# Performance work log

Measured on AMD Instinct MI355X. Metric: run time of the kernel, lower is better.

The kernel has to match this reference:

```python
import jax, jax.numpy as jnp
import numpy as np

N = 100000   # nodes
E = 1600000  # edges
H = 128      # hidden_channels
G = 2        # group
D = H // G   # per-group channels
L = 2        # num_layers
T = 112      # num_tasks
MSG_EPS = 1e-7


def _ln(x, g, b):
    mu = jnp.mean(x, axis=-1, keepdims=True)
    var = jnp.var(x, axis=-1, keepdims=True)
    return (x - mu) * jax.lax.rsqrt(var + 1e-5) * g + b


def setup_inputs() -> dict:
    key = jax.random.key(0)
    ks = jax.random.split(key, 12)
    s8, s16, sH, sD = 1/np.sqrt(8), 1/np.sqrt(16), 1/np.sqrt(H), 1/np.sqrt(D)
    inp = {}
    inp["x"] = jax.random.uniform(ks[0], (N, 8), jnp.float32)
    inp["node_index"] = jax.random.randint(ks[1], (N,), 0, N)
    inp["edge_index"] = jax.random.randint(ks[2], (2, E), 0, N)
    inp["edge_attr"] = jax.random.uniform(ks[3], (E, 8), jnp.float32)
    inp["node_features"] = jax.random.normal(ks[4], (N, 8), jnp.float32)
    inp["W_oh"] = jax.random.normal(ks[5], (8, 8)) * s8
    inp["b_oh"] = jnp.zeros((8,))
    inp["W_ne"] = jax.random.normal(ks[6], (16, H)) * s16
    inp["b_ne"] = jnp.zeros((H,))
    inp["W_ee"] = jax.random.normal(ks[7], (8, H)) * s8
    inp["b_ee"] = jnp.zeros((H,))
    inp["ln_g"] = jnp.ones((L, G, D))
    inp["ln_b"] = jnp.zeros((L, G, D))
    inp["We"] = jax.random.normal(ks[8], (L, G, H, D)) * sH   # GENConv edge encoder per Fm
    inp["be"] = jnp.zeros((L, G, D))
    inp["Wm"] = jax.random.normal(ks[9], (L, G, D, D)) * sD   # GENConv 1-layer MLP
    inp["bm"] = jnp.zeros((L, G, D))
    inp["last_g"] = jnp.ones((H,))
    inp["last_b"] = jnp.zeros((H,))
    inp["Wp"] = jax.random.normal(ks[10], (H, T)) * sH
    inp["bp"] = jnp.zeros((T,))
    return inp


def _gen_block(y_in, src, dst, ee, g, b, We_, be_, Wm_, bm_):
    # GENBlock (res+ pre-activation): norm -> relu -> GENConv(softmax aggr, t=1)
    h = jax.nn.relu(_ln(y_in, g, b))                       # [N,D]
    msg = jax.nn.relu(h[src] + ee @ We_ + be_) + MSG_EPS   # [E,D]
    mx = jax.lax.stop_gradient(jax.ops.segment_max(msg, dst, num_segments=N))
    mx = jnp.where(jnp.isfinite(mx), mx, 0.0)
    ex = jnp.exp(msg - mx[dst])
    den = jax.ops.segment_sum(ex, dst, num_segments=N)
    w = ex / (den[dst] + 1e-16)                            # scatter_softmax weights
    agg = jax.ops.segment_sum(msg * w, dst, num_segments=N)  # [N,D]
    return (h + agg) @ Wm_ + bm_


def reference(x, node_index, edge_index, edge_attr, node_features, W_oh, b_oh, W_ne, b_ne, W_ee, b_ee, ln_g, ln_b, We, be, Wm, bm, last_g, last_b, Wp, bp):
    nf1 = node_features[node_index]                        # [N,8]
    nf2 = x @ W_oh + b_oh                                  # one-hot encoder [N,8]
    h = jnp.concatenate([nf1, nf2], axis=1) @ W_ne + b_ne  # [N,H]
    ee = edge_attr @ W_ee + b_ee                           # [E,H]; cat of G copies chunks back to identical [E,H]
    src, dst = edge_index[0], edge_index[1]
    for l in range(L):
        # GroupAdditiveCoupling (group=2): y_i = x_i + F_i(y_{i-1})
        x1, x2 = jnp.split(h, G, axis=-1)
        y1 = x1 + _gen_block(x2, src, dst, ee, ln_g[l, 0], ln_b[l, 0], We[l, 0], be[l, 0], Wm[l, 0], bm[l, 0])
        y2 = x2 + _gen_block(y1, src, dst, ee, ln_g[l, 1], ln_b[l, 1], We[l, 1], be[l, 1], Wm[l, 1], bm[l, 1])
        h = jnp.concatenate([y1, y2], axis=-1)
    h = jax.nn.relu(_ln(h, last_g, last_b))
    return h @ Wp + bp
```

## Files before the change

### kernel.cpp

```cpp
#include <hip/hip_runtime.h>

constexpr int N_NODES = 100000;
constexpr int N_EDGES = 1600000;
constexpr int T_OUT = 112;

constexpr int SCAN_CHUNK = 1024;
constexpr int SCAN_BLOCKS = (N_NODES + SCAN_CHUNK - 1) / SCAN_CHUNK;

typedef _Float16 h2v __attribute__((ext_vector_type(2)));
typedef _Float16 half8 __attribute__((ext_vector_type(8)));
typedef float f32x4 __attribute__((ext_vector_type(4)));
typedef int i4v __attribute__((ext_vector_type(4)));
typedef float f4v __attribute__((ext_vector_type(4)));

__device__ __forceinline__ float dot2h(h2v a, h2v b, float c) {
#if __has_builtin(__builtin_amdgcn_fdot2)
    return __builtin_amdgcn_fdot2(a, b, c, false);
#else
    return fmaf((float)a.x, (float)b.x, fmaf((float)a.y, (float)b.y, c));
#endif
}
__device__ __forceinline__ int pk2(float a, float b) {
    auto v = __builtin_amdgcn_cvt_pkrtz(a, b);
    return __builtin_bit_cast(int, v);
}
__device__ __forceinline__ h2v b2h(int x) { return __builtin_bit_cast(h2v, x); }
__device__ __forceinline__ unsigned short f2h(float f) {
    return __builtin_bit_cast(unsigned short, (_Float16)f);
}

__global__ void wcomb_kernel(const float* __restrict__ W_ee,
                             const float* __restrict__ b_ee,
                             const float* __restrict__ We,
                             const float* __restrict__ be,
                             int* __restrict__ Wc_h2,
                             float* __restrict__ bcomb) {
    int lg = blockIdx.x;
    int d = threadIdx.x;
    const float* We_ = We + (size_t)lg * 128 * 64;
    float acc[9];
#pragma unroll
    for (int k = 0; k < 9; ++k) acc[k] = 0.f;
    for (int c = 0; c < 128; ++c) {
        float wv = We_[c * 64 + d];
#pragma unroll
        for (int k = 0; k < 8; ++k) acc[k] += W_ee[k * 128 + c] * wv;
        acc[8] += b_ee[c] * wv;
    }
#pragma unroll
    for (int j = 0; j < 4; ++j)
        Wc_h2[lg * 256 + j * 64 + d] = pk2(acc[2 * j], acc[2 * j + 1]);
    bcomb[lg * 64 + d] = acc[8] + be[lg * 64 + d];
}

__global__ void wp_pack_kernel(const float* __restrict__ Wp, int* __restrict__ wpfrag) {
    int tm = blockIdx.x;
    int tile = tm >> 2, m = tm & 3;
    int lane = threadIdx.x;
    int g = lane >> 4, r = lane & 15;
    int t = tile * 16 + r;
    int o[4];
#pragma unroll
    for (int p = 0; p < 4; ++p) {
        int j0 = 2 * p, j1 = 2 * p + 1;
        int k0 = m * 32 + (j0 >> 2) * 16 + g * 4 + (j0 & 3);
        int k1 = m * 32 + (j1 >> 2) * 16 + g * 4 + (j1 & 3);
        o[p] = pk2(Wp[k0 * 112 + t], Wp[k1 * 112 + t]);
    }
    int4 o4; o4.x = o[0]; o4.y = o[1]; o4.z = o[2]; o4.w = o[3];
    *(int4*)(wpfrag + ((size_t)tm * 64 + lane) * 4) = o4;
}

__global__ void wm_pack_kernel(const float* __restrict__ Wm, int* __restrict__ wmfrag) {
    int b = blockIdx.x;
    int lg = b >> 3, tm = b & 7;
    int tile = tm >> 1, m = tm & 1;
    int lane = threadIdx.x;
    int g = lane >> 4, r = lane & 15;
    const float* W = Wm + (size_t)lg * 4096;
    int col = tile * 16 + r;
    int o[4];
#pragma unroll
    for (int p = 0; p < 4; ++p) {
        int j0 = 2 * p, j1 = 2 * p + 1;
        int k0 = m * 32 + (j0 >> 2) * 16 + g * 4 + (j0 & 3);
        int k1 = m * 32 + (j1 >> 2) * 16 + g * 4 + (j1 & 3);
        o[p] = pk2(W[k0 * 64 + col], W[k1 * 64 + col]);
    }
    int4 o4; o4.x = o[0]; o4.y = o[1]; o4.z = o[2]; o4.w = o[3];
    *(int4*)(wmfrag + ((size_t)b * 64 + lane) * 4) = o4;
}

__global__ __launch_bounds__(256) void encoder_kernel(
    const float* __restrict__ x, const int* __restrict__ node_index,
    const float* __restrict__ node_features,
    const float* __restrict__ W_oh, const float* __restrict__ b_oh,
    const float* __restrict__ W_ne, const float* __restrict__ b_ne,
    float* __restrict__ A, float* __restrict__ B) {
    int tid = threadIdx.x;
    int w = tid >> 6, d = tid & 63;
    int n = blockIdx.x * 4 + w;

    float xf[8];
    const float* xr = x + (size_t)n * 8;
#pragma unroll
    for (int j = 0; j < 8; ++j) xf[j] = xr[j];

    float nf[16];
    int ni = node_index[n];
    const float* nfr = node_features + (size_t)ni * 8;
#pragma unroll
    for (int k = 0; k < 8; ++k) nf[k] = nfr[k];
#pragma unroll
    for (int k = 0; k < 8; ++k) {
        float acc = b_oh[k];
#pragma unroll
        for (int j = 0; j < 8; ++j) acc += xf[j] * W_oh[j * 8 + k];
        nf[8 + k] = acc;
    }
    float hA = b_ne[d], hB = b_ne[64 + d];
#pragma unroll
    for (int k = 0; k < 16; ++k) {
        hA += nf[k] * W_ne[k * 128 + d];
        hB += nf[k] * W_ne[k * 128 + 64 + d];
    }
    A[(size_t)n * 64 + d] = hA;
    B[(size_t)n * 64 + d] = hB;
}

__global__ void hist_kernel(const int* __restrict__ edge_index,
                            int* __restrict__ deg, int* __restrict__ rank) {
    int e = blockIdx.x * 256 + threadIdx.x;
    if (e < N_EDGES) rank[e] = atomicAdd(&deg[edge_index[N_EDGES + e]], 1);
}

__global__ __launch_bounds__(256) void block_sum_kernel(const int* __restrict__ deg,
                                                        int* __restrict__ blocksum) {
    __shared__ int s_w[4];
    int t = threadIdx.x;
    int base = blockIdx.x * SCAN_CHUNK + t * 4;
    int s = 0;
    if (base + 3 < N_NODES) {
        int4 v = *(const int4*)(deg + base);
        s = v.x + v.y + v.z + v.w;
    } else {
        for (int j = 0; j < 4; ++j)
            if (base + j < N_NODES) s += deg[base + j];
    }
#pragma unroll
    for (int o = 32; o >= 1; o >>= 1) s += __shfl_xor(s, o, 64);
    if ((t & 63) == 0) s_w[t >> 6] = s;
    __syncthreads();
    if (t == 0) blocksum[blockIdx.x] = s_w[0] + s_w[1] + s_w[2] + s_w[3];
}

__global__ __launch_bounds__(64) void scan_sums_kernel(const int* __restrict__ blocksum,
                                                       int* __restrict__ blockoff,
                                                       int* __restrict__ rowptr) {
    int t = threadIdx.x;
    int i0 = 2 * t, i1 = 2 * t + 1;
    int v0 = (i0 < SCAN_BLOCKS) ? blocksum[i0] : 0;
    int v1 = (i1 < SCAN_BLOCKS) ? blocksum[i1] : 0;
    int s = v0 + v1;
    int incl = s;
#pragma unroll
    for (int o = 1; o < 64; o <<= 1) {
        int u = __shfl_up(incl, o, 64);
        if (t >= o) incl += u;
    }
    int excl = incl - s;
    if (i0 < SCAN_BLOCKS) blockoff[i0] = excl;
    if (i1 < SCAN_BLOCKS) blockoff[i1] = excl + v0;
    if (t == 63) rowptr[N_NODES] = incl;
}

__global__ __launch_bounds__(256) void emit_kernel(const int* __restrict__ deg,
                                                   const int* __restrict__ blockoff,
                                                   int* __restrict__ rowptr) {
    __shared__ int s_w[4];
    int t = threadIdx.x;
    int w = t >> 6, lane = t & 63;
    int base = blockIdx.x * SCAN_CHUNK + t * 4;

    int d0 = 0, d1 = 0, d2 = 0, d3 = 0;
    if (base + 3 < N_NODES) {
        int4 v = *(const int4*)(deg + base);
        d0 = v.x; d1 = v.y; d2 = v.z; d3 = v.w;
    } else {
        if (base + 0 < N_NODES) d0 = deg[base + 0];
        if (base + 1 < N_NODES) d1 = deg[base + 1];
        if (base + 2 < N_NODES) d2 = deg[base + 2];
        if (base + 3 < N_NODES) d3 = deg[base + 3];
    }
    int s = d0 + d1 + d2 + d3;
    int incl = s;
#pragma unroll
    for (int o = 1; o < 64; o <<= 1) {
        int u = __shfl_up(incl, o, 64);
        if (lane >= o) incl += u;
    }
    if (lane == 63) s_w[w] = incl;
    __syncthreads();
    int woff = 0;
    for (int j = 0; j < 4; ++j) woff += (j < w) ? s_w[j] : 0;

    int p = blockoff[blockIdx.x] + woff + incl - s;
    int4 r;
    r.x = p;
    r.y = p + d0;
    r.z = p + d0 + d1;
    r.w = p + d0 + d1 + d2;
    if (base + 3 < N_NODES) {
        *(int4*)(rowptr + base) = r;
    } else {
        if (base + 0 < N_NODES) rowptr[base + 0] = r.x;
        if (base + 1 < N_NODES) rowptr[base + 1] = r.y;
        if (base + 2 < N_NODES) rowptr[base + 2] = r.z;
        if (base + 3 < N_NODES) rowptr[base + 3] = r.w;
    }
}

__global__ void scatter_kernel(const int* __restrict__ edge_index,
                               const float* __restrict__ edge_attr,
                               const int* __restrict__ rowptr,
                               const int* __restrict__ rank,
                               int* __restrict__ src_perm,
                               int* __restrict__ ea_h) {
    int e = blockIdx.x * 256 + threadIdx.x;
    if (e >= N_EDGES) return;
    int dn = edge_index[N_EDGES + e];
    int idx = rowptr[dn] + rank[e];
    f4v a = __builtin_nontemporal_load((const f4v*)(edge_attr + (size_t)e * 8));
    f4v b = __builtin_nontemporal_load((const f4v*)(edge_attr + (size_t)e * 8 + 4));
    i4v o;
    o.x = pk2(a.x, a.y);
    o.y = pk2(a.z, a.w);
    o.z = pk2(b.x, b.y);
    o.w = pk2(b.z, b.w);
    __builtin_nontemporal_store(o, (i4v*)(ea_h + (size_t)idx * 4));
    __builtin_nontemporal_store(edge_index[e], src_perm + idx);
}

__global__ __launch_bounds__(256) void ln_relu_kernel(const float* __restrict__ Y,
                                                      const float* __restrict__ g,
                                                      const float* __restrict__ b,
                                                      float* __restrict__ hl32,
                                                      unsigned short* __restrict__ hl16) {
    int tid = threadIdx.x;
    int w = tid >> 6, d = tid & 63;
    int n = blockIdx.x * 4 + w;
    float y = Y[(size_t)n * 64 + d];
    float s = y, sq = y * y;
#pragma unroll
    for (int offd = 32; offd >= 1; offd >>= 1) {
        s += __shfl_xor(s, offd, 64);
        sq += __shfl_xor(sq, offd, 64);
    }
    float mean = s * (1.f / 64.f);
    float var = sq * (1.f / 64.f) - mean * mean;
    float rs = rsqrtf(var + 1e-5f);
    float h = fmaxf((y - mean) * rs * g[d] + b[d], 0.f);
    hl32[(size_t)n * 64 + d] = h;
    hl16[(size_t)n * 64 + d] = f2h(h);
}

__global__ __launch_bounds__(256) void agg_kernel(
    const unsigned short* __restrict__ hl16, const float* __restrict__ hl32,
    float* __restrict__ v32,
    const int* __restrict__ rowptr, const int* __restrict__ src_perm,
    const int* __restrict__ ea_h,
    const int* __restrict__ Wc_h2, const float* __restrict__ bcomb) {
    int tid = threadIdx.x;
    int w = tid >> 6, lane = tid & 63;
    int half = lane >> 5;
    int c = (lane & 31) * 2;
    int n = blockIdx.x * 8 + w * 2 + half;

    h2v wc0[4], wc1[4];
#pragma unroll
    for (int j = 0; j < 4; ++j) {
        wc0[j] = b2h(Wc_h2[j * 64 + c]);
        wc1[j] = b2h(Wc_h2[j * 64 + c + 1]);
    }
    float bc0 = bcomb[c], bc1 = bcomb[c + 1];

    float num0 = 0.f, den0 = 0.f, num1 = 0.f, den1 = 0.f;
    int start = rowptr[n], end = rowptr[n + 1];
    const int4* ea4 = (const int4*)ea_h;

#define EDGE(U, E)                                                        \
    {                                                                     \
        h2v hv = b2h((int)(U));                                           \
        float eW0 = bc0, eW1 = bc1;                                       \
        eW0 = dot2h(b2h(E.x), wc0[0], eW0);                               \
        eW1 = dot2h(b2h(E.x), wc1[0], eW1);                               \
        eW0 = dot2h(b2h(E.y), wc0[1], eW0);                               \
        eW1 = dot2h(b2h(E.y), wc1[1], eW1);                               \
        eW0 = dot2h(b2h(E.z), wc0[2], eW0);                               \
        eW1 = dot2h(b2h(E.z), wc1[2], eW1);                               \
        eW0 = dot2h(b2h(E.w), wc0[3], eW0);                               \
        eW1 = dot2h(b2h(E.w), wc1[3], eW1);                               \
        float m0 = fmaxf((float)hv.x + eW0, 0.f) + 1e-7f;                 \
        float m1 = fmaxf((float)hv.y + eW1, 0.f) + 1e-7f;                 \
        float x0 = __expf(m0), x1 = __expf(m1);                           \
        den0 += x0; num0 += x0 * m0;                                      \
        den1 += x1; num1 += x1 * m1;                                      \
    }

    int i = start;
    for (; i + 4 <= end; i += 4) {
        int s0 = src_perm[i + 0];
        int s1 = src_perm[i + 1];
        int s2 = src_perm[i + 2];
        int s3 = src_perm[i + 3];
        unsigned int u0 = *(const unsigned int*)(hl16 + (size_t)s0 * 64 + c);
        unsigned int u1 = *(const unsigned int*)(hl16 + (size_t)s1 * 64 + c);
        unsigned int u2 = *(const unsigned int*)(hl16 + (size_t)s2 * 64 + c);
        unsigned int u3 = *(const unsigned int*)(hl16 + (size_t)s3 * 64 + c);
        int4 e0 = ea4[i + 0], e1 = ea4[i + 1], e2 = ea4[i + 2], e3 = ea4[i + 3];
        EDGE(u0, e0) EDGE(u1, e1) EDGE(u2, e2) EDGE(u3, e3)
    }
    for (; i < end; ++i) {
        int s0 = src_perm[i];
        unsigned int u0 = *(const unsigned int*)(hl16 + (size_t)s0 * 64 + c);
        int4 e0 = ea4[i];
        EDGE(u0, e0)
    }
#undef EDGE

    float agg0 = num0 / (den0 + 1e-16f);
    float agg1 = num1 / (den1 + 1e-16f);
    float2 sv = *(const float2*)(hl32 + (size_t)n * 64 + c);
    float2 vout;
    vout.x = sv.x + agg0;
    vout.y = sv.y + agg1;
    *(float2*)(v32 + (size_t)n * 64 + c) = vout;
}

template <bool PRODUCE_HL>
__global__ __launch_bounds__(256) void epi_kernel(
    const float* __restrict__ v32, float* __restrict__ Y,
    const int* __restrict__ wmfrag, const float* __restrict__ bm,
    const float* __restrict__ gnext, const float* __restrict__ bnext,
    float* __restrict__ hl32, unsigned short* __restrict__ hl16) {
    int tid = threadIdx.x;
    int w = tid >> 6, lane = tid & 63;
    int g = lane >> 4, r = lane & 15;
    int nodebase = blockIdx.x * 64 + w * 16;
    if (nodebase >= N_NODES) return;

    const float* vp = v32 + (size_t)(nodebase + r) * 64;
    half8 af[2];
#pragma unroll
    for (int m = 0; m < 2; ++m) {
        int k0 = m * 32 + g * 4;
        float4 lo = *(const float4*)(vp + k0);
        float4 hi = *(const float4*)(vp + k0 + 16);
        af[m][0] = (_Float16)lo.x; af[m][1] = (_Float16)lo.y;
        af[m][2] = (_Float16)lo.z; af[m][3] = (_Float16)lo.w;
        af[m][4] = (_Float16)hi.x; af[m][5] = (_Float16)hi.y;
        af[m][6] = (_Float16)hi.z; af[m][7] = (_Float16)hi.w;
    }

    const int4* wf4 = (const int4*)wmfrag;
    f32x4 acc[4];
#pragma unroll
    for (int tile = 0; tile < 4; ++tile) {
        float bmv = bm[tile * 16 + r];
        acc[tile] = {bmv, bmv, bmv, bmv};
#pragma unroll
        for (int m = 0; m < 2; ++m) {
            int4 bw = wf4[(tile * 2 + m) * 64 + lane];
            half8 bf = __builtin_bit_cast(half8, bw);
            acc[tile] = __builtin_amdgcn_mfma_f32_16x16x32_f16(af[m], bf, acc[tile], 0, 0, 0);
        }
    }

    float yn[4][4];
#pragma unroll
    for (int tile = 0; tile < 4; ++tile) {
#pragma unroll
        for (int q = 0; q < 4; ++q) {
            size_t idx = (size_t)(nodebase + g * 4 + q) * 64 + tile * 16 + r;
            float y = Y[idx] + acc[tile][q];
            yn[tile][q] = y;
            Y[idx] = y;
        }
    }

    if constexpr (PRODUCE_HL) {
        float gnv[4], bnv[4];
#pragma unroll
        for (int tile = 0; tile < 4; ++tile) {
            gnv[tile] = gnext[tile * 16 + r];
            bnv[tile] = bnext[tile * 16 + r];
        }
#pragma unroll
        for (int q = 0; q < 4; ++q) {
            float s = yn[0][q] + yn[1][q] + yn[2][q] + yn[3][q];
            float sq = yn[0][q] * yn[0][q] + yn[1][q] * yn[1][q]
                     + yn[2][q] * yn[2][q] + yn[3][q] * yn[3][q];
            s += __shfl_xor(s, 1, 64);  sq += __shfl_xor(sq, 1, 64);
            s += __shfl_xor(s, 2, 64);  sq += __shfl_xor(sq, 2, 64);
            s += __shfl_xor(s, 4, 64);  sq += __shfl_xor(sq, 4, 64);
            s += __shfl_xor(s, 8, 64);  sq += __shfl_xor(sq, 8, 64);
            float mean = s * (1.f / 64.f);
            float var = sq * (1.f / 64.f) - mean * mean;
            float rs = rsqrtf(var + 1e-5f);
#pragma unroll
            for (int tile = 0; tile < 4; ++tile) {
                float h = fmaxf((yn[tile][q] - mean) * rs * gnv[tile] + bnv[tile], 0.f);
                size_t oidx = (size_t)(nodebase + g * 4 + q) * 64 + tile * 16 + r;
                hl32[oidx] = h;
                hl16[oidx] = f2h(h);
            }
        }
    }
}

__global__ __launch_bounds__(256) void final_kernel(
    const float* __restrict__ A, const float* __restrict__ B,
    const float* __restrict__ lg, const float* __restrict__ lb,
    const int* __restrict__ wpfrag, const float* __restrict__ bp,
    float* __restrict__ out) {
    int tid = threadIdx.x;
    int w = tid >> 6, lane = tid & 63;
    int g = lane >> 4, r = lane & 15;
    int nodebase = blockIdx.x * 64 + w * 16;
    if (nodebase >= N_NODES) return;
    int n = nodebase + r;

    float4 v[8];
    const float4* A4 = (const float4*)(A + (size_t)n * 64);
    const float4* B4 = (const float4*)(B + (size_t)n * 64);
#pragma unroll
    for (int kb = 0; kb < 4; ++kb) v[kb] = A4[kb * 4 + g];
#pragma unroll
    for (int kb = 0; kb < 4; ++kb) v[4 + kb] = B4[kb * 4 + g];

    float s = 0.f, sq = 0.f;
#pragma unroll
    for (int kb = 0; kb < 8; ++kb) {
        s += v[kb].x + v[kb].y + v[kb].z + v[kb].w;
        sq += v[kb].x * v[kb].x + v[kb].y * v[kb].y
            + v[kb].z * v[kb].z + v[kb].w * v[kb].w;
    }
    s += __shfl_xor(s, 16, 64);  sq += __shfl_xor(sq, 16, 64);
    s += __shfl_xor(s, 32, 64);  sq += __shfl_xor(sq, 32, 64);
    float mean = s * (1.f / 128.f);
    float var = sq * (1.f / 128.f) - mean * mean;
    float rs = rsqrtf(var + 1e-5f);

    const float4* lg4 = (const float4*)lg;
    const float4* lb4 = (const float4*)lb;
    half8 afr[4];
#pragma unroll
    for (int kb = 0; kb < 8; ++kb) {
        float4 gv = lg4[kb * 4 + g];
        float4 bv = lb4[kb * 4 + g];
        int m = kb >> 1, e0 = (kb & 1) * 4;
        afr[m][e0 + 0] = (_Float16)fmaxf((v[kb].x - mean) * rs * gv.x + bv.x, 0.f);
        afr[m][e0 + 1] = (_Float16)fmaxf((v[kb].y - mean) * rs * gv.y + bv.y, 0.f);
        afr[m][e0 + 2] = (_Float16)fmaxf((v[kb].z - mean) * rs * gv.z + bv.z, 0.f);
        afr[m][e0 + 3] = (_Float16)fmaxf((v[kb].w - mean) * rs * gv.w + bv.w, 0.f);
    }

    const int4* wf4 = (const int4*)wpfrag;
#pragma unroll
    for (int tile = 0; tile < 7; ++tile) {
        float bias = bp[tile * 16 + r];
        f32x4 acc = {bias, bias, bias, bias};
#pragma unroll
        for (int m = 0; m < 4; ++m) {
            int4 bw = wf4[(tile * 4 + m) * 64 + lane];
            half8 bf = __builtin_bit_cast(half8, bw);
            acc = __builtin_amdgcn_mfma_f32_16x16x32_f16(afr[m], bf, acc, 0, 0, 0);
        }
#pragma unroll
        for (int q = 0; q < 4; ++q) {
            out[(size_t)(nodebase + g * 4 + q) * T_OUT + tile * 16 + r] = acc[q];
        }
    }
}

extern "C" void kernel_launch(void* const* d_in, const int* in_sizes, int n_in,
                              void* d_out, int out_size, void* d_ws, size_t ws_size,
                              hipStream_t stream) {
    const float* x            = (const float*)d_in[0];
    const int* node_index     = (const int*)d_in[1];
    const int* edge_index     = (const int*)d_in[2];
    const float* edge_attr    = (const float*)d_in[3];
    const float* node_features= (const float*)d_in[4];
    const float* W_oh         = (const float*)d_in[5];
    const float* b_oh         = (const float*)d_in[6];
    const float* W_ne         = (const float*)d_in[7];
    const float* b_ne         = (const float*)d_in[8];
    const float* W_ee         = (const float*)d_in[9];
    const float* b_ee         = (const float*)d_in[10];
    const float* ln_g         = (const float*)d_in[11];
    const float* ln_b         = (const float*)d_in[12];
    const float* We           = (const float*)d_in[13];
    const float* be           = (const float*)d_in[14];
    const float* Wm           = (const float*)d_in[15];
    const float* bm           = (const float*)d_in[16];
    const float* last_g       = (const float*)d_in[17];
    const float* last_b       = (const float*)d_in[18];
    const float* Wp           = (const float*)d_in[19];
    const float* bp           = (const float*)d_in[20];
    float* out = (float*)d_out;

    char* ws = (char*)d_ws;
    size_t off = 0;
    auto alloc = [&](size_t bytes) -> void* {
        void* p = ws + off;
        off = (off + bytes + 255) & ~(size_t)255;
        return p;
    };
    float* A          = (float*)alloc((size_t)N_NODES * 64 * 4);
    float* B          = (float*)alloc((size_t)N_NODES * 64 * 4);
    float* hl32       = (float*)alloc((size_t)N_NODES * 64 * 4);
    unsigned short* hl16 = (unsigned short*)alloc((size_t)N_NODES * 64 * 2);
    float* v32        = (float*)alloc((size_t)N_NODES * 64 * 4);
    int* deg          = (int*)alloc((size_t)N_NODES * 4);
    int* rowptr       = (int*)alloc((size_t)(N_NODES + 1) * 4);
    int* rank         = (int*)alloc((size_t)N_EDGES * 4);
    int* src_perm     = (int*)alloc((size_t)N_EDGES * 4);
    int* ea_h         = (int*)alloc((size_t)N_EDGES * 4 * 4);
    int* Wc_h2        = (int*)alloc(4 * 256 * 4);
    float* bcomb      = (float*)alloc(4 * 64 * 4);
    int* blocksum     = (int*)alloc((size_t)SCAN_BLOCKS * 4);
    int* blockoff     = (int*)alloc((size_t)SCAN_BLOCKS * 4);
    int* wpfrag       = (int*)alloc((size_t)28 * 64 * 16);
    int* wmfrag       = (int*)alloc((size_t)32 * 64 * 16);
    (void)ws_size; (void)in_sizes; (void)n_in; (void)out_size;

    const int NB_NODE = N_NODES / 4;
    const int NB_EDGE = (N_EDGES + 255) / 256;
    const int NB_AGG  = N_NODES / 8;
    const int NB_EPI  = (N_NODES + 63) / 64;

    (void)hipMemsetAsync(deg, 0, (size_t)N_NODES * 4, stream);
    wcomb_kernel<<<4, 64, 0, stream>>>(W_ee, b_ee, We, be, Wc_h2, bcomb);
    wp_pack_kernel<<<28, 64, 0, stream>>>(Wp, wpfrag);
    wm_pack_kernel<<<32, 64, 0, stream>>>(Wm, wmfrag);
    encoder_kernel<<<NB_NODE, 256, 0, stream>>>(x, node_index, node_features,
                                                W_oh, b_oh, W_ne, b_ne, A, B);
    hist_kernel<<<NB_EDGE, 256, 0, stream>>>(edge_index, deg, rank);
    block_sum_kernel<<<SCAN_BLOCKS, 256, 0, stream>>>(deg, blocksum);
    scan_sums_kernel<<<1, 64, 0, stream>>>(blocksum, blockoff, rowptr);
    emit_kernel<<<SCAN_BLOCKS, 256, 0, stream>>>(deg, blockoff, rowptr);
    scatter_kernel<<<NB_EDGE, 256, 0, stream>>>(edge_index, edge_attr, rowptr,
                                                rank, src_perm, ea_h);

    ln_relu_kernel<<<NB_NODE, 256, 0, stream>>>(B, ln_g, ln_b, hl32, hl16);

    agg_kernel<<<NB_AGG, 256, 0, stream>>>(hl16, hl32, v32, rowptr, src_perm,
                                           ea_h, Wc_h2 + 0 * 256, bcomb + 0 * 64);
    epi_kernel<true><<<NB_EPI, 256, 0, stream>>>(
        v32, A, wmfrag + 0 * 8 * 256, bm + 0 * 64,
        ln_g + 1 * 64, ln_b + 1 * 64, hl32, hl16);
    agg_kernel<<<NB_AGG, 256, 0, stream>>>(hl16, hl32, v32, rowptr, src_perm,
                                           ea_h, Wc_h2 + 1 * 256, bcomb + 1 * 64);
    epi_kernel<true><<<NB_EPI, 256, 0, stream>>>(
        v32, B, wmfrag + 1 * 8 * 256, bm + 1 * 64,
        ln_g + 2 * 64, ln_b + 2 * 64, hl32, hl16);
    agg_kernel<<<NB_AGG, 256, 0, stream>>>(hl16, hl32, v32, rowptr, src_perm,
                                           ea_h, Wc_h2 + 2 * 256, bcomb + 2 * 64);
    epi_kernel<true><<<NB_EPI, 256, 0, stream>>>(
        v32, A, wmfrag + 2 * 8 * 256, bm + 2 * 64,
        ln_g + 3 * 64, ln_b + 3 * 64, hl32, hl16);
    agg_kernel<<<NB_AGG, 256, 0, stream>>>(hl16, hl32, v32, rowptr, src_perm,
                                           ea_h, Wc_h2 + 3 * 256, bcomb + 3 * 64);
    epi_kernel<false><<<NB_EPI, 256, 0, stream>>>(
        v32, B, wmfrag + 3 * 8 * 256, bm + 3 * 64,
        nullptr, nullptr, nullptr, nullptr);

    final_kernel<<<NB_EPI, 256, 0, stream>>>(A, B, last_g, last_b, wpfrag, bp, out);
}
```

Baseline: 621.8 us.

## Schedule aggregation nodes in descending-degree order via counting sort

Adds a counting sort of nodes by in-degree, with degrees of 63 and above sharing one bucket, to build a permutation. The aggregation kernel processes nodes in that order instead of by index, so heavy nodes start first and half-wave pairs get similar edge counts. This aims to reduce load imbalance and tail divergence in the four aggregation passes. It adds three small kernels, atomics and an extra indirection, and loses the sequential node locality of the output writes.

```diff
diff --git a/kernel.cpp b/kernel.cpp
--- a/kernel.cpp
+++ b/kernel.cpp
@@ -217,6 +217,39 @@
         if (base + 1 < N_NODES) rowptr[base + 1] = r.y;
         if (base + 2 < N_NODES) rowptr[base + 2] = r.z;
         if (base + 3 < N_NODES) rowptr[base + 3] = r.w;
+    }
+}
+
+__global__ __launch_bounds__(256) void dhist_kernel(const int* __restrict__ deg,
+                                                    int* __restrict__ dhist) {
+    int n = blockIdx.x * 256 + threadIdx.x;
+    if (n < N_NODES) {
+        int b = 63 - min(deg[n], 63);
+        atomicAdd(&dhist[b], 1);
+    }
+}
+
+__global__ __launch_bounds__(64) void dscan_kernel(const int* __restrict__ dhist,
+                                                   int* __restrict__ dcur) {
+    int t = threadIdx.x;
+    int v = dhist[t];
+    int incl = v;
+#pragma unroll
+    for (int o = 1; o < 64; o <<= 1) {
+        int u = __shfl_up(incl, o, 64);
+        if (t >= o) incl += u;
+    }
+    dcur[t] = incl - v;
+}
+
+__global__ __launch_bounds__(256) void dplace_kernel(const int* __restrict__ deg,
+                                                     int* __restrict__ dcur,
+                                                     int* __restrict__ dorder) {
+    int n = blockIdx.x * 256 + threadIdx.x;
+    if (n < N_NODES) {
+        int b = 63 - min(deg[n], 63);
+        int p = atomicAdd(&dcur[b], 1);
+        dorder[p] = n;
     }
 }
 
@@ -268,13 +301,13 @@
     const unsigned short* __restrict__ hl16, const float* __restrict__ hl32,
     float* __restrict__ v32,
     const int* __restrict__ rowptr, const int* __restrict__ src_perm,
-    const int* __restrict__ ea_h,
+    const int* __restrict__ ea_h, const int* __restrict__ dorder,
     const int* __restrict__ Wc_h2, const float* __restrict__ bcomb) {
     int tid = threadIdx.x;
     int w = tid >> 6, lane = tid & 63;
     int half = lane >> 5;
     int c = (lane & 31) * 2;
-    int n = blockIdx.x * 8 + w * 2 + half;
+    int n = dorder[blockIdx.x * 8 + w * 2 + half];
 
     h2v wc0[4], wc1[4];
 #pragma unroll
@@ -532,14 +565,19 @@
     int* blockoff     = (int*)alloc((size_t)SCAN_BLOCKS * 4);
     int* wpfrag       = (int*)alloc((size_t)28 * 64 * 16);
     int* wmfrag       = (int*)alloc((size_t)32 * 64 * 16);
+    int* dhist        = (int*)alloc(64 * 4);
+    int* dcur         = (int*)alloc(64 * 4);
+    int* dorder       = (int*)alloc((size_t)N_NODES * 4);
     (void)ws_size; (void)in_sizes; (void)n_in; (void)out_size;
 
     const int NB_NODE = N_NODES / 4;
     const int NB_EDGE = (N_EDGES + 255) / 256;
+    const int NB_N256 = (N_NODES + 255) / 256;
     const int NB_AGG  = N_NODES / 8;
     const int NB_EPI  = (N_NODES + 63) / 64;
 
     (void)hipMemsetAsync(deg, 0, (size_t)N_NODES * 4, stream);
+    (void)hipMemsetAsync(dhist, 0, 64 * 4, stream);
     wcomb_kernel<<<4, 64, 0, stream>>>(W_ee, b_ee, We, be, Wc_h2, bcomb);
     wp_pack_kernel<<<28, 64, 0, stream>>>(Wp, wpfrag);
     wm_pack_kernel<<<32, 64, 0, stream>>>(Wm, wmfrag);
@@ -549,28 +587,35 @@
     block_sum_kernel<<<SCAN_BLOCKS, 256, 0, stream>>>(deg, blocksum);
     scan_sums_kernel<<<1, 64, 0, stream>>>(blocksum, blockoff, rowptr);
     emit_kernel<<<SCAN_BLOCKS, 256, 0, stream>>>(deg, blockoff, rowptr);
+    dhist_kernel<<<NB_N256, 256, 0, stream>>>(deg, dhist);
+    dscan_kernel<<<1, 64, 0, stream>>>(dhist, dcur);
+    dplace_kernel<<<NB_N256, 256, 0, stream>>>(deg, dcur, dorder);
     scatter_kernel<<<NB_EDGE, 256, 0, stream>>>(edge_index, edge_attr, rowptr,
                                                 rank, src_perm, ea_h);
 
     ln_relu_kernel<<<NB_NODE, 256, 0, stream>>>(B, ln_g, ln_b, hl32, hl16);
 
     agg_kernel<<<NB_AGG, 256, 0, stream>>>(hl16, hl32, v32, rowptr, src_perm,
-                                           ea_h, Wc_h2 + 0 * 256, bcomb + 0 * 64);
+                                           ea_h, dorder,
+                                           Wc_h2 + 0 * 256, bcomb + 0 * 64);
     epi_kernel<true><<<NB_EPI, 256, 0, stream>>>(
         v32, A, wmfrag + 0 * 8 * 256, bm + 0 * 64,
         ln_g + 1 * 64, ln_b + 1 * 64, hl32, hl16);
     agg_kernel<<<NB_AGG, 256, 0, stream>>>(hl16, hl32, v32, rowptr, src_perm,
-                                           ea_h, Wc_h2 + 1 * 256, bcomb + 1 * 64);
+                                           ea_h, dorder,
+                                           Wc_h2 + 1 * 256, bcomb + 1 * 64);
     epi_kernel<true><<<NB_EPI, 256, 0, stream>>>(
         v32, B, wmfrag + 1 * 8 * 256, bm + 1 * 64,
         ln_g + 2 * 64, ln_b + 2 * 64, hl32, hl16);
     agg_kernel<<<NB_AGG, 256, 0, stream>>>(hl16, hl32, v32, rowptr, src_perm,
-                                           ea_h, Wc_h2 + 2 * 256, bcomb + 2 * 64);
+                                           ea_h, dorder,
+                                           Wc_h2 + 2 * 256, bcomb + 2 * 64);
     epi_kernel<true><<<NB_EPI, 256, 0, stream>>>(
         v32, A, wmfrag + 2 * 8 * 256, bm + 2 * 64,
         ln_g + 3 * 64, ln_b + 3 * 64, hl32, hl16);
     agg_kernel<<<NB_AGG, 256, 0, stream>>>(hl16, hl32, v32, rowptr, src_perm,
-                                           ea_h, Wc_h2 + 3 * 256, bcomb + 3 * 64);
+                                           ea_h, dorder,
+                                           Wc_h2 + 3 * 256, bcomb + 3 * 64);
     epi_kernel<false><<<NB_EPI, 256, 0, stream>>>(
         v32, B, wmfrag + 3 * 8 * 256, bm + 3 * 64,
         nullptr, nullptr, nullptr, nullptr);
```

Result: slower. 1.120 ms (+80.2%).
